# Performance work log

Hardware: AMD Instinct MI355X
Metric: run time of the kernel (lower is better)

## Reference

```python
import jax, jax.numpy as jnp
import numpy as np

B, N, D, H = 256, 196, 384, 1536  # batch, patches, dim, mlp hidden


def fake_quant(w, bits):
    """Symmetric per-tensor uniform fake quantization with straight-through estimator."""
    qmax = 2.0 ** (bits - 1) - 1.0
    scale = jnp.maximum(jnp.max(jnp.abs(w)) / qmax, 1e-8)
    q = jnp.clip(jnp.round(w / scale), -qmax, qmax) * scale
    return w + jax.lax.stop_gradient(q - w)


def setup_inputs() -> dict:
    key = jax.random.key(0)
    ks = jax.random.split(key, 8)
    return {
        "x": jax.random.normal(ks[0], (B, N, D), jnp.float32),
        "alpha1": jnp.ones((D,), jnp.float32),
        "beta1": jnp.zeros((D,), jnp.float32),
        "W_attn": jax.random.normal(ks[1], (N, N), jnp.float32) * (1.0 / np.sqrt(N)),
        "b_attn": jnp.zeros((N,), jnp.float32),
        "gamma1": jax.random.uniform(ks[2], (D,), jnp.float32) * 0.1,
        "alpha2": jnp.ones((D,), jnp.float32),
        "beta2": jnp.zeros((D,), jnp.float32),
        "W1": jax.random.normal(ks[3], (H, D), jnp.float32) * (1.0 / np.sqrt(D)),
        "b1": jnp.zeros((H,), jnp.float32),
        "W2": jax.random.normal(ks[4], (D, H), jnp.float32) * (1.0 / np.sqrt(H)),
        "b2": jnp.zeros((D,), jnp.float32),
        "gamma2": jax.random.uniform(ks[5], (D,), jnp.float32) * 0.1,
        "bits": 8,
    }


def reference(x, alpha1, beta1, W_attn, b_attn, gamma1,
              alpha2, beta2, W1, b1, W2, b2, gamma2, bits):
    # --- token-mixing branch ---
    org = x
    h = alpha1 * x + beta1                                   # Aff norm1, [B,N,D]
    # transpose(1,2) -> [B,D,N]; Linear(N,N); transpose back == einsum over patch dim
    Wq = fake_quant(W_attn, bits)
    h = jnp.einsum('bnd,mn->bmd', h, Wq) + b_attn[:, None]   # [B,N,D], bias per patch
    x = gamma1 * h + org                                     # layerscale + residual
    # --- channel-mixing branch ---
    org = x
    h = alpha2 * x + beta2                                   # Aff norm2
    h = jax.nn.gelu(h @ fake_quant(W1, bits).T + b1)         # [B,N,H]
    h = h @ fake_quant(W2, bits).T + b2                      # [B,N,D]
    return gamma2 * h + org
```

## Files before the change

### kernel.cpp

```cpp
#include <hip/hip_runtime.h>
#include <hip/hip_bf16.h>
#include <stdint.h>

#define Bb 256
#define Nn 196
#define Dd 384
#define Hh 1536
#define NPAD 224
#define MPAD 256
#define TTOT (Bb*Nn)
#define XLD 232

typedef __attribute__((ext_vector_type(8))) __bf16 bf16x8;
typedef __attribute__((ext_vector_type(4))) float f32x4;

#define GLD16(gp, lp) __builtin_amdgcn_global_load_lds( \
    (const __attribute__((address_space(1))) void*)(gp), \
    (__attribute__((address_space(3))) void*)(lp), 16, 0, 0)

__device__ __forceinline__ ushort f2bf(float f){
  union { float f; unsigned u; } v; v.f = f;
  unsigned r = v.u + 0x7FFFu + ((v.u >> 16) & 1u);
  return (ushort)(r >> 16);
}

__global__ void absmax_k(const float* __restrict__ w, int n, unsigned* __restrict__ out){
  float m = 0.f;
  for (int i = blockIdx.x*blockDim.x + threadIdx.x; i < n; i += gridDim.x*blockDim.x)
    m = fmaxf(m, fabsf(w[i]));
  #pragma unroll
  for (int o = 32; o >= 1; o >>= 1) m = fmaxf(m, __shfl_xor(m, o));
  __shared__ float sm[4];
  if ((threadIdx.x & 63) == 0) sm[threadIdx.x >> 6] = m;
  __syncthreads();
  if (threadIdx.x == 0){
    float mm = fmaxf(fmaxf(sm[0], sm[1]), fmaxf(sm[2], sm[3]));
    atomicMax(out, __float_as_uint(mm));
  }
}

__global__ void quant_attn_k(const float* __restrict__ W, const unsigned* __restrict__ amax,
                             const int* __restrict__ bitsp, ushort* __restrict__ Wq){
  int idx = blockIdx.x*256 + threadIdx.x;
  int m = idx / NPAD, n = idx - m*NPAD;
  float qmax = (float)((1 << (bitsp[0]-1)) - 1);
  float s = fmaxf(__uint_as_float(amax[0]) / qmax, 1e-8f);
  float v = 0.f;
  if (m < Nn && n < Nn){
    float q = fminf(fmaxf(rintf(W[m*Nn + n] / s), -qmax), qmax);
    v = q * s;
  }
  Wq[idx] = f2bf(v);
}

__global__ void quant_k(const float* __restrict__ W, int n, const unsigned* __restrict__ amax,
                        const int* __restrict__ bitsp, ushort* __restrict__ Wq){
  int idx = blockIdx.x*256 + threadIdx.x;
  if (idx >= n) return;
  float qmax = (float)((1 << (bitsp[0]-1)) - 1);
  float s = fmaxf(__uint_as_float(amax[0]) / qmax, 1e-8f);
  float q = fminf(fmaxf(rintf(W[idx] / s), -qmax), qmax);
  Wq[idx] = f2bf(q * s);
}

__device__ __forceinline__ void stage_tile(const ushort* __restrict__ src, long ld, int k0,
                                           ushort* dst){
  const int tid = threadIdx.x;
  const long row = tid >> 2;
  const int  c8  = (tid & 3) * 8;
  GLD16(src + row*ld + k0 + c8,        dst + tid*8);
  GLD16(src + (row+64)*ld + k0 + c8,   dst + 2048 + tid*8);
}

__device__ __forceinline__ void gemm_core_gl(const ushort* __restrict__ A, long ldA,
                                             const ushort* __restrict__ B, long ldB,
                                             int K, ushort* As, ushort* Bs, f32x4 acc[4][4]){
  const int tid  = threadIdx.x;
  const int lane = tid & 63;
  const int wr   = (tid >> 7) & 1;
  const int wc   = (tid >> 6) & 1;
  const int arow = lane & 15;
  const int koff = (lane >> 4) * 8;
  for (int k0 = 0; k0 < K; k0 += 32){
    __syncthreads();
    stage_tile(A, ldA, k0, As);
    stage_tile(B, ldB, k0, Bs);
    __syncthreads();
    bf16x8 ag[4], bg[4];
    #pragma unroll
    for (int i=0;i<4;i++){
      ag[i] = *(const bf16x8*)&As[(wr*64 + i*16 + arow)*32 + koff];
      bg[i] = *(const bf16x8*)&Bs[(wc*64 + i*16 + arow)*32 + koff];
    }
    #pragma unroll
    for (int i=0;i<4;i++)
      #pragma unroll
      for (int j=0;j<4;j++)
        acc[i][j] = __builtin_amdgcn_mfma_f32_16x16x32_bf16(ag[i], bg[j], acc[i][j], 0, 0, 0);
  }
}

__global__ __launch_bounds__(256) void gemm1_k(const ushort* __restrict__ Wq,
    const float* __restrict__ x,
    const float* __restrict__ alpha1, const float* __restrict__ beta1,
    const float* __restrict__ b_attn, const float* __restrict__ gamma1,
    const float* __restrict__ alpha2, const float* __restrict__ beta2,
    float* __restrict__ x1, ushort* __restrict__ hn2){
  __shared__ ushort Xs[128*XLD];
  __shared__ ushort BufAs[8192];
  const int tid = threadIdx.x;
  const int b = blockIdx.y, dt = blockIdx.x, d0 = dt*128;

  {
    float* buf = (float*)BufAs;
    const int dme = tid & 127;
    const float a1 = alpha1[d0 + dme], be1 = beta1[d0 + dme];
    for (int p = 0; p < 7; p++){
      __syncthreads();
      #pragma unroll
      for (int c = 0; c < 4; c++){
        int nn = p*32 + c*8 + (tid >> 5);
        int ncl = nn < Nn ? nn : Nn - 1;
        GLD16(x + ((long)b*Nn + ncl)*Dd + d0 + (tid & 31)*4,
              (char*)BufAs + c*4096 + tid*16);
      }
      __syncthreads();
      for (int g = tid >> 7; g < 4; g += 2){
        int n0 = g*8;
        ushort o[8];
        #pragma unroll
        for (int t = 0; t < 8; t++){
          int na = p*32 + n0 + t;
          float val = (na < Nn) ? fmaf(a1, buf[(n0 + t)*128 + dme], be1) : 0.f;
          o[t] = f2bf(val);
        }
        *(int4*)&Xs[dme*XLD + p*32 + n0] = *(int4*)o;
      }
    }
  }

  const int lane = tid & 63;
  const int wr = (tid >> 7) & 1, wc = (tid >> 6) & 1;
  const int arow = lane & 15, koff = (lane >> 4)*8;
  ushort* As = BufAs;
  for (int mt = 0; mt < 2; mt++){
    f32x4 acc[4][4] = {};
    const ushort* Wt = Wq + (long)mt*128*NPAD;
    for (int k0 = 0; k0 < NPAD; k0 += 32){
      __syncthreads();
      stage_tile(Wt, NPAD, k0, As);
      __syncthreads();
      bf16x8 ag[4], bg[4];
      #pragma unroll
      for (int i=0;i<4;i++){
        ag[i] = *(const bf16x8*)&As[(wr*64 + i*16 + arow)*32 + koff];
        bg[i] = *(const bf16x8*)&Xs[(wc*64 + i*16 + arow)*XLD + k0 + koff];
      }
      #pragma unroll
      for (int i=0;i<4;i++)
        #pragma unroll
        for (int j=0;j<4;j++)
          acc[i][j] = __builtin_amdgcn_mfma_f32_16x16x32_bf16(ag[i], bg[j], acc[i][j], 0, 0, 0);
    }
    #pragma unroll
    for (int i=0;i<4;i++){
      #pragma unroll
      for (int j=0;j<4;j++){
        int d = d0 + wc*64 + j*16 + (lane & 15);
        float g1 = gamma1[d], a2 = alpha2[d], b2v = beta2[d];
        #pragma unroll
        for (int r=0;r<4;r++){
          int m = mt*128 + wr*64 + i*16 + (lane >> 4)*4 + r;
          if (m < Nn){
            long idx = ((long)b*Nn + m)*Dd + d;
            float o = fmaf(g1, acc[i][j][r] + b_attn[m], x[idx]);
            x1[idx]  = o;
            hn2[idx] = f2bf(fmaf(a2, o, b2v));
          }
        }
      }
    }
  }
}

__global__ __launch_bounds__(256) void gemm2_k(const ushort* __restrict__ hn2,
    const ushort* __restrict__ W1q, const float* __restrict__ b1,
    ushort* __restrict__ h2, int t0){
  __shared__ ushort As[4096];
  __shared__ ushort Bs[4096];
  int ht = blockIdx.x, tt = blockIdx.y;
  f32x4 acc[4][4] = {};
  gemm_core_gl(hn2 + ((long)t0 + tt*128)*Dd, Dd, W1q + (long)ht*128*Dd, Dd, Dd, As, Bs, acc);
  int lane = threadIdx.x & 63;
  int wr = (threadIdx.x >> 7) & 1, wc = (threadIdx.x >> 6) & 1;
  #pragma unroll
  for (int i=0;i<4;i++){
    #pragma unroll
    for (int j=0;j<4;j++){
      int h = ht*128 + wc*64 + j*16 + (lane & 15);
      float bias = b1[h];
      #pragma unroll
      for (int r=0;r<4;r++){
        int t = tt*128 + wr*64 + i*16 + (lane >> 4)*4 + r;
        float v = acc[i][j][r] + bias;
        float u = 0.7978845608028654f * v * fmaf(0.044715f, v*v, 1.f);
        float g = v / (1.f + __expf(-2.f*u));
        h2[(long)t*Hh + h] = f2bf(g);
      }
    }
  }
}

__global__ __launch_bounds__(256) void gemm3_k(const ushort* __restrict__ h2,
    const ushort* __restrict__ W2q, const float* __restrict__ b2,
    const float* __restrict__ gamma2, float* __restrict__ out, int t0){
  __shared__ ushort As[4096];
  __shared__ ushort Bs[4096];
  int dt = blockIdx.x, tt = blockIdx.y;
  f32x4 acc[4][4] = {};
  gemm_core_gl(h2 + (long)tt*128*Hh, Hh, W2q + (long)dt*128*Hh, Hh, Hh, As, Bs, acc);
  int lane = threadIdx.x & 63;
  int wr = (threadIdx.x >> 7) & 1, wc = (threadIdx.x >> 6) & 1;
  #pragma unroll
  for (int i=0;i<4;i++){
    #pragma unroll
    for (int j=0;j<4;j++){
      int d = dt*128 + wc*64 + j*16 + (lane & 15);
      float g2 = gamma2[d], bias = b2[d];
      #pragma unroll
      for (int r=0;r<4;r++){
        long t = (long)t0 + tt*128 + wr*64 + i*16 + (lane >> 4)*4 + r;
        long idx = t*Dd + d;
        out[idx] = fmaf(g2, acc[i][j][r] + bias, out[idx]);
      }
    }
  }
}

extern "C" void kernel_launch(void* const* d_in, const int* in_sizes, int n_in,
                              void* d_out, int out_size, void* d_ws, size_t ws_size,
                              hipStream_t stream){
  const float* x      = (const float*)d_in[0];
  const float* alpha1 = (const float*)d_in[1];
  const float* beta1  = (const float*)d_in[2];
  const float* W_attn = (const float*)d_in[3];
  const float* b_attn = (const float*)d_in[4];
  const float* gamma1 = (const float*)d_in[5];
  const float* alpha2 = (const float*)d_in[6];
  const float* beta2  = (const float*)d_in[7];
  const float* W1     = (const float*)d_in[8];
  const float* b1     = (const float*)d_in[9];
  const float* W2     = (const float*)d_in[10];
  const float* b2     = (const float*)d_in[11];
  const float* gamma2 = (const float*)d_in[12];
  const int*   bits   = (const int*)d_in[13];

  char* ws = (char*)d_ws;
  unsigned* amax = (unsigned*)ws;
  ushort* Wq   = (ushort*)(ws + 256);
  ushort* W1q  = (ushort*)(ws + 114944);
  ushort* W2q  = (ushort*)(ws + 1294592);
  ushort* hn2  = (ushort*)(ws + 2474240);
  ushort* h2   = (ushort*)(ws + 41009408);
  float*  x1   = (float*)d_out;

  const size_t fixed_end = 41009408ull;
  int nchunk;
  if      (ws_size >= fixed_end + 154140672ull) nchunk = 1;
  else if (ws_size >= fixed_end +  77070336ull) nchunk = 2;
  else                                          nchunk = 4;
  const int TC = TTOT / nchunk;

  hipMemsetAsync(amax, 0, 256, stream);
  absmax_k<<<128, 256, 0, stream>>>(W_attn, Nn*Nn, amax + 0);
  absmax_k<<<256, 256, 0, stream>>>(W1, Hh*Dd, amax + 1);
  absmax_k<<<256, 256, 0, stream>>>(W2, Hh*Dd, amax + 2);
  quant_attn_k<<<(MPAD*NPAD)/256, 256, 0, stream>>>(W_attn, amax, bits, Wq);
  quant_k<<<(Hh*Dd)/256, 256, 0, stream>>>(W1, Hh*Dd, amax + 1, bits, W1q);
  quant_k<<<(Hh*Dd)/256, 256, 0, stream>>>(W2, Hh*Dd, amax + 2, bits, W2q);
  gemm1_k<<<dim3(3, Bb), 256, 0, stream>>>(Wq, x, alpha1, beta1, b_attn, gamma1,
                                           alpha2, beta2, x1, hn2);
  for (int c = 0; c < nchunk; c++){
    gemm2_k<<<dim3(Hh/128, TC/128), 256, 0, stream>>>(hn2, W1q, b1, h2, c*TC);
    gemm3_k<<<dim3(Dd/128, TC/128), 256, 0, stream>>>(h2, W2q, b2, gamma2,
                                                      (float*)d_out, c*TC);
  }
}
```

Measured before the change: 401.5 us.

## Merge quant kernels, swap GEMM operands for vectorized epilogues, read Wq from global in gemm1

Folds the three absmax launches into one and the three quantize launches into one, using blockIdx.y to select the tensor. The GEMM operands are swapped so each lane holds four consecutive feature columns, which lets the epilogues of gemm1, gemm2 and gemm3 use float4 and int2 stores instead of strided scalar ones. gemm1 now reads the quantized attention weight straight from global or cache instead of staging it in LDS, adds a launch-bounds occupancy hint, and drops the per-k barriers. The chunk count is fixed at 2 instead of depending on workspace size, which risks overflow if the workspace is too small for half the hidden buffer.

```diff
diff --git a/kernel.cpp b/kernel.cpp
--- a/kernel.cpp
+++ b/kernel.cpp
@@ -10,6 +10,7 @@
 #define MPAD 256
 #define TTOT (Bb*Nn)
 #define XLD 232
+#define TC 25088
 
 typedef __attribute__((ext_vector_type(8))) __bf16 bf16x8;
 typedef __attribute__((ext_vector_type(4))) float f32x4;
@@ -17,6 +18,8 @@
 #define GLD16(gp, lp) __builtin_amdgcn_global_load_lds( \
     (const __attribute__((address_space(1))) void*)(gp), \
     (__attribute__((address_space(3))) void*)(lp), 16, 0, 0)
+
+#define MFMA16(a, b, c) __builtin_amdgcn_mfma_f32_16x16x32_bf16((a), (b), (c), 0, 0, 0)
 
 __device__ __forceinline__ ushort f2bf(float f){
   union { float f; unsigned u; } v; v.f = f;
@@ -24,7 +27,11 @@
   return (ushort)(r >> 16);
 }
 
-__global__ void absmax_k(const float* __restrict__ w, int n, unsigned* __restrict__ out){
+__global__ void absmax3_k(const float* __restrict__ wa, const float* __restrict__ w1,
+                          const float* __restrict__ w2, unsigned* __restrict__ out){
+  int which = blockIdx.y;
+  const float* w = which == 0 ? wa : (which == 1 ? w1 : w2);
+  int n = which == 0 ? Nn*Nn : Hh*Dd;
   float m = 0.f;
   for (int i = blockIdx.x*blockDim.x + threadIdx.x; i < n; i += gridDim.x*blockDim.x)
     m = fmaxf(m, fabsf(w[i]));
@@ -35,32 +42,34 @@
   __syncthreads();
   if (threadIdx.x == 0){
     float mm = fmaxf(fmaxf(sm[0], sm[1]), fmaxf(sm[2], sm[3]));
-    atomicMax(out, __float_as_uint(mm));
-  }
-}
-
-__global__ void quant_attn_k(const float* __restrict__ W, const unsigned* __restrict__ amax,
-                             const int* __restrict__ bitsp, ushort* __restrict__ Wq){
-  int idx = blockIdx.x*256 + threadIdx.x;
-  int m = idx / NPAD, n = idx - m*NPAD;
-  float qmax = (float)((1 << (bitsp[0]-1)) - 1);
-  float s = fmaxf(__uint_as_float(amax[0]) / qmax, 1e-8f);
-  float v = 0.f;
-  if (m < Nn && n < Nn){
-    float q = fminf(fmaxf(rintf(W[m*Nn + n] / s), -qmax), qmax);
-    v = q * s;
-  }
-  Wq[idx] = f2bf(v);
-}
-
-__global__ void quant_k(const float* __restrict__ W, int n, const unsigned* __restrict__ amax,
-                        const int* __restrict__ bitsp, ushort* __restrict__ Wq){
-  int idx = blockIdx.x*256 + threadIdx.x;
-  if (idx >= n) return;
-  float qmax = (float)((1 << (bitsp[0]-1)) - 1);
-  float s = fmaxf(__uint_as_float(amax[0]) / qmax, 1e-8f);
-  float q = fminf(fmaxf(rintf(W[idx] / s), -qmax), qmax);
-  Wq[idx] = f2bf(q * s);
+    atomicMax(out + which, __float_as_uint(mm));
+  }
+}
+
+__global__ void quant_all_k(const float* __restrict__ Wa, const float* __restrict__ W1,
+                            const float* __restrict__ W2, const unsigned* __restrict__ amax,
+                            const int* __restrict__ bitsp,
+                            ushort* __restrict__ Wq, ushort* __restrict__ W1q,
+                            ushort* __restrict__ W2q){
+  const int which = blockIdx.y;
+  const int idx = blockIdx.x*256 + threadIdx.x;
+  const float qmax = (float)((1 << (bitsp[0]-1)) - 1);
+  const float s = fmaxf(__uint_as_float(amax[which]) / qmax, 1e-8f);
+  if (which == 0){
+    if (idx >= MPAD*NPAD) return;
+    int m = idx / NPAD, n = idx - m*NPAD;
+    float v = 0.f;
+    if (m < Nn && n < Nn){
+      float q = fminf(fmaxf(rintf(Wa[m*Nn + n] / s), -qmax), qmax);
+      v = q * s;
+    }
+    Wq[idx] = f2bf(v);
+  } else {
+    const float* W = (which == 1) ? W1 : W2;
+    ushort* Wo = (which == 1) ? W1q : W2q;
+    float q = fminf(fmaxf(rintf(W[idx] / s), -qmax), qmax);
+    Wo[idx] = f2bf(q * s);
+  }
 }
 
 __device__ __forceinline__ void stage_tile(const ushort* __restrict__ src, long ld, int k0,
@@ -96,23 +105,22 @@
     for (int i=0;i<4;i++)
       #pragma unroll
       for (int j=0;j<4;j++)
-        acc[i][j] = __builtin_amdgcn_mfma_f32_16x16x32_bf16(ag[i], bg[j], acc[i][j], 0, 0, 0);
-  }
-}
-
-__global__ __launch_bounds__(256) void gemm1_k(const ushort* __restrict__ Wq,
+        acc[i][j] = MFMA16(ag[i], bg[j], acc[i][j]);
+  }
+}
+
+__global__ __launch_bounds__(256, 2) void gemm1_k(const ushort* __restrict__ Wq,
     const float* __restrict__ x,
     const float* __restrict__ alpha1, const float* __restrict__ beta1,
     const float* __restrict__ b_attn, const float* __restrict__ gamma1,
     const float* __restrict__ alpha2, const float* __restrict__ beta2,
     float* __restrict__ x1, ushort* __restrict__ hn2){
   __shared__ ushort Xs[128*XLD];
-  __shared__ ushort BufAs[8192];
+  __shared__ float  Sbuf[32*128];
   const int tid = threadIdx.x;
   const int b = blockIdx.y, dt = blockIdx.x, d0 = dt*128;
 
   {
-    float* buf = (float*)BufAs;
     const int dme = tid & 127;
     const float a1 = alpha1[d0 + dme], be1 = beta1[d0 + dme];
     for (int p = 0; p < 7; p++){
@@ -122,7 +130,7 @@
         int nn = p*32 + c*8 + (tid >> 5);
         int ncl = nn < Nn ? nn : Nn - 1;
         GLD16(x + ((long)b*Nn + ncl)*Dd + d0 + (tid & 31)*4,
-              (char*)BufAs + c*4096 + tid*16);
+              (char*)Sbuf + c*4096 + tid*16);
       }
       __syncthreads();
       for (int g = tid >> 7; g < 4; g += 2){
@@ -131,52 +139,61 @@
         #pragma unroll
         for (int t = 0; t < 8; t++){
           int na = p*32 + n0 + t;
-          float val = (na < Nn) ? fmaf(a1, buf[(n0 + t)*128 + dme], be1) : 0.f;
+          float val = (na < Nn) ? fmaf(a1, Sbuf[(n0 + t)*128 + dme], be1) : 0.f;
           o[t] = f2bf(val);
         }
         *(int4*)&Xs[dme*XLD + p*32 + n0] = *(int4*)o;
       }
     }
   }
+  __syncthreads();
 
   const int lane = tid & 63;
   const int wr = (tid >> 7) & 1, wc = (tid >> 6) & 1;
   const int arow = lane & 15, koff = (lane >> 4)*8;
-  ushort* As = BufAs;
+  const int g = lane >> 4;
   for (int mt = 0; mt < 2; mt++){
     f32x4 acc[4][4] = {};
-    const ushort* Wt = Wq + (long)mt*128*NPAD;
-    for (int k0 = 0; k0 < NPAD; k0 += 32){
-      __syncthreads();
-      stage_tile(Wt, NPAD, k0, As);
-      __syncthreads();
+    #pragma unroll
+    for (int k7 = 0; k7 < 7; k7++){
       bf16x8 ag[4], bg[4];
       #pragma unroll
       for (int i=0;i<4;i++){
-        ag[i] = *(const bf16x8*)&As[(wr*64 + i*16 + arow)*32 + koff];
-        bg[i] = *(const bf16x8*)&Xs[(wc*64 + i*16 + arow)*XLD + k0 + koff];
+        int row = mt*128 + wr*64 + i*16 + arow;
+        ag[i] = *(const bf16x8*)&Wq[row*NPAD + k7*32 + koff];
+        bg[i] = *(const bf16x8*)&Xs[(wc*64 + i*16 + arow)*XLD + k7*32 + koff];
       }
       #pragma unroll
       for (int i=0;i<4;i++)
         #pragma unroll
         for (int j=0;j<4;j++)
-          acc[i][j] = __builtin_amdgcn_mfma_f32_16x16x32_bf16(ag[i], bg[j], acc[i][j], 0, 0, 0);
+          acc[i][j] = MFMA16(bg[i], ag[j], acc[i][j]);
     }
     #pragma unroll
     for (int i=0;i<4;i++){
+      const int d = d0 + wc*64 + i*16 + g*4;
+      const float4 g1 = *(const float4*)&gamma1[d];
+      const float4 a2 = *(const float4*)&alpha2[d];
+      const float4 b2v = *(const float4*)&beta2[d];
       #pragma unroll
       for (int j=0;j<4;j++){
-        int d = d0 + wc*64 + j*16 + (lane & 15);
-        float g1 = gamma1[d], a2 = alpha2[d], b2v = beta2[d];
-        #pragma unroll
-        for (int r=0;r<4;r++){
-          int m = mt*128 + wr*64 + i*16 + (lane >> 4)*4 + r;
-          if (m < Nn){
-            long idx = ((long)b*Nn + m)*Dd + d;
-            float o = fmaf(g1, acc[i][j][r] + b_attn[m], x[idx]);
-            x1[idx]  = o;
-            hn2[idx] = f2bf(fmaf(a2, o, b2v));
-          }
+        const int m = mt*128 + wr*64 + j*16 + arow;
+        if (m < Nn){
+          const long base = ((long)b*Nn + m)*Dd + d;
+          const float4 xv = *(const float4*)&x[base];
+          const float ba = b_attn[m];
+          float4 o;
+          o.x = fmaf(g1.x, acc[i][j][0] + ba, xv.x);
+          o.y = fmaf(g1.y, acc[i][j][1] + ba, xv.y);
+          o.z = fmaf(g1.z, acc[i][j][2] + ba, xv.z);
+          o.w = fmaf(g1.w, acc[i][j][3] + ba, xv.w);
+          *(float4*)&x1[base] = o;
+          ushort h4[4];
+          h4[0] = f2bf(fmaf(a2.x, o.x, b2v.x));
+          h4[1] = f2bf(fmaf(a2.y, o.y, b2v.y));
+          h4[2] = f2bf(fmaf(a2.z, o.z, b2v.z));
+          h4[3] = f2bf(fmaf(a2.w, o.w, b2v.w));
+          *(int2*)&hn2[base] = *(int2*)h4;
         }
       }
     }
@@ -185,54 +202,63 @@
 
 __global__ __launch_bounds__(256) void gemm2_k(const ushort* __restrict__ hn2,
     const ushort* __restrict__ W1q, const float* __restrict__ b1,
-    ushort* __restrict__ h2, int t0){
+    ushort* __restrict__ h2, int t0c){
   __shared__ ushort As[4096];
   __shared__ ushort Bs[4096];
-  int ht = blockIdx.x, tt = blockIdx.y;
+  const int ht = blockIdx.x, tt = blockIdx.y;
+  const long t0 = (long)t0c + tt*128;
   f32x4 acc[4][4] = {};
-  gemm_core_gl(hn2 + ((long)t0 + tt*128)*Dd, Dd, W1q + (long)ht*128*Dd, Dd, Dd, As, Bs, acc);
-  int lane = threadIdx.x & 63;
-  int wr = (threadIdx.x >> 7) & 1, wc = (threadIdx.x >> 6) & 1;
+  gemm_core_gl(W1q + (long)ht*128*Dd, Dd, hn2 + t0*Dd, Dd, Dd, As, Bs, acc);
+  const int lane = threadIdx.x & 63;
+  const int wr = (threadIdx.x >> 7) & 1, wc = (threadIdx.x >> 6) & 1;
+  const int arow = lane & 15, g = lane >> 4;
   #pragma unroll
   for (int i=0;i<4;i++){
+    const int h0 = ht*128 + wr*64 + i*16 + g*4;
+    const float4 b1v = *(const float4*)&b1[h0];
     #pragma unroll
     for (int j=0;j<4;j++){
-      int h = ht*128 + wc*64 + j*16 + (lane & 15);
-      float bias = b1[h];
+      const long tok = t0 + wc*64 + j*16 + arow;
+      ushort h4[4];
       #pragma unroll
       for (int r=0;r<4;r++){
-        int t = tt*128 + wr*64 + i*16 + (lane >> 4)*4 + r;
-        float v = acc[i][j][r] + bias;
+        float v = acc[i][j][r] + ((const float*)&b1v)[r];
         float u = 0.7978845608028654f * v * fmaf(0.044715f, v*v, 1.f);
-        float g = v / (1.f + __expf(-2.f*u));
-        h2[(long)t*Hh + h] = f2bf(g);
-      }
+        float gl = v / (1.f + __expf(-2.f*u));
+        h4[r] = f2bf(gl);
+      }
+      *(int2*)&h2[tok*Hh + h0] = *(int2*)h4;
     }
   }
 }
 
 __global__ __launch_bounds__(256) void gemm3_k(const ushort* __restrict__ h2,
     const ushort* __restrict__ W2q, const float* __restrict__ b2,
-    const float* __restrict__ gamma2, float* __restrict__ out, int t0){
+    const float* __restrict__ gamma2, float* __restrict__ out, int t0c){
   __shared__ ushort As[4096];
   __shared__ ushort Bs[4096];
-  int dt = blockIdx.x, tt = blockIdx.y;
+  const int dt = blockIdx.x, tt = blockIdx.y;
+  const long t0 = (long)t0c + tt*128;
   f32x4 acc[4][4] = {};
-  gemm_core_gl(h2 + (long)tt*128*Hh, Hh, W2q + (long)dt*128*Hh, Hh, Hh, As, Bs, acc);
-  int lane = threadIdx.x & 63;
-  int wr = (threadIdx.x >> 7) & 1, wc = (threadIdx.x >> 6) & 1;
+  gemm_core_gl(W2q + (long)dt*128*Hh, Hh, h2 + t0*Hh, Hh, Hh, As, Bs, acc);
+  const int lane = threadIdx.x & 63;
+  const int wr = (threadIdx.x >> 7) & 1, wc = (threadIdx.x >> 6) & 1;
+  const int arow = lane & 15, g = lane >> 4;
   #pragma unroll
   for (int i=0;i<4;i++){
+    const int d = dt*128 + wr*64 + i*16 + g*4;
+    const float4 g2 = *(const float4*)&gamma2[d];
+    const float4 bv = *(const float4*)&b2[d];
     #pragma unroll
     for (int j=0;j<4;j++){
-      int d = dt*128 + wc*64 + j*16 + (lane & 15);
-      float g2 = gamma2[d], bias = b2[d];
-      #pragma unroll
-      for (int r=0;r<4;r++){
-        long t = (long)t0 + tt*128 + wr*64 + i*16 + (lane >> 4)*4 + r;
-        long idx = t*Dd + d;
-        out[idx] = fmaf(g2, acc[i][j][r] + bias, out[idx]);
-      }
+      const long tok = t0 + wc*64 + j*16 + arow;
+      const long base = tok*Dd + d;
+      float4 o = *(const float4*)&out[base];
+      o.x = fmaf(g2.x, acc[i][j][0] + bv.x, o.x);
+      o.y = fmaf(g2.y, acc[i][j][1] + bv.y, o.y);
+      o.z = fmaf(g2.z, acc[i][j][2] + bv.z, o.z);
+      o.w = fmaf(g2.w, acc[i][j][3] + bv.w, o.w);
+      *(float4*)&out[base] = o;
     }
   }
 }
@@ -264,23 +290,13 @@
   ushort* h2   = (ushort*)(ws + 41009408);
   float*  x1   = (float*)d_out;
 
-  const size_t fixed_end = 41009408ull;
-  int nchunk;
-  if      (ws_size >= fixed_end + 154140672ull) nchunk = 1;
-  else if (ws_size >= fixed_end +  77070336ull) nchunk = 2;
-  else                                          nchunk = 4;
-  const int TC = TTOT / nchunk;
-
   hipMemsetAsync(amax, 0, 256, stream);
-  absmax_k<<<128, 256, 0, stream>>>(W_attn, Nn*Nn, amax + 0);
-  absmax_k<<<256, 256, 0, stream>>>(W1, Hh*Dd, amax + 1);
-  absmax_k<<<256, 256, 0, stream>>>(W2, Hh*Dd, amax + 2);
-  quant_attn_k<<<(MPAD*NPAD)/256, 256, 0, stream>>>(W_attn, amax, bits, Wq);
-  quant_k<<<(Hh*Dd)/256, 256, 0, stream>>>(W1, Hh*Dd, amax + 1, bits, W1q);
-  quant_k<<<(Hh*Dd)/256, 256, 0, stream>>>(W2, Hh*Dd, amax + 2, bits, W2q);
+  absmax3_k<<<dim3(128, 3), 256, 0, stream>>>(W_attn, W1, W2, amax);
+  quant_all_k<<<dim3((Hh*Dd)/256, 3), 256, 0, stream>>>(W_attn, W1, W2, amax, bits,
+                                                        Wq, W1q, W2q);
   gemm1_k<<<dim3(3, Bb), 256, 0, stream>>>(Wq, x, alpha1, beta1, b_attn, gamma1,
                                            alpha2, beta2, x1, hn2);
-  for (int c = 0; c < nchunk; c++){
+  for (int c = 0; c < 2; c++){
     gemm2_k<<<dim3(Hh/128, TC/128), 256, 0, stream>>>(hn2, W1q, b1, h2, c*TC);
     gemm3_k<<<dim3(Dd/128, TC/128), 256, 0, stream>>>(h2, W2q, b2, gamma2,
                                                       (float*)d_out, c*TC);
```

Result: no change. 407.4 us (+1.5%).
